# Kernel tuning notes

Measured on AMD Instinct MI355X. Metric: run time of the kernel, lower is better.

Reference implementation:

```python
import jax, jax.numpy as jnp
import numpy as np

NODES = 14      # input_size: nodes per graph
IN_F = 24       # seq_len: node feature dim
HID1 = 32
HID2 = 64       # hid_feats
HEADS = 2
OUT = 24        # output_size
B = 2048        # number of graphs
SLOPE = 0.2


def _make_edges():
    # fully connected (no self loops) within each 14-node graph
    pairs = np.array([(i, j) for i in range(NODES) for j in range(NODES) if i != j]).T  # [2,182]
    offs = (np.arange(B) * NODES)[:, None]
    src = (pairs[0][None, :] + offs).reshape(-1)
    dst = (pairs[1][None, :] + offs).reshape(-1)
    return np.stack([src, dst]).astype(np.int32)  # [2, 372736]


def setup_inputs() -> dict:
    key = jax.random.key(0)
    ks = jax.random.split(key, 16)
    N = B * NODES
    x = jax.random.normal(ks[0], (N, IN_F), dtype=jnp.float32)
    y = jax.random.normal(ks[1], (N, OUT), dtype=jnp.float32)
    edge_index = jnp.asarray(_make_edges())
    batch = jnp.repeat(jnp.arange(B, dtype=jnp.int32), NODES)
    s = 0.1
    params = dict(
        W1=jax.random.normal(ks[2], (IN_F, HEADS * HID1), dtype=jnp.float32) * s,
        a_src1=jax.random.normal(ks[3], (HEADS, HID1), dtype=jnp.float32) * s,
        a_dst1=jax.random.normal(ks[4], (HEADS, HID1), dtype=jnp.float32) * s,
        b1=jnp.zeros((HID1,), dtype=jnp.float32),
        W2=jax.random.normal(ks[5], (HID1, HEADS * HID2), dtype=jnp.float32) * s,
        a_src2=jax.random.normal(ks[6], (HEADS, HID2), dtype=jnp.float32) * s,
        a_dst2=jax.random.normal(ks[7], (HEADS, HID2), dtype=jnp.float32) * s,
        b2=jnp.zeros((HID2,), dtype=jnp.float32),
        Wf1=jax.random.normal(ks[8], (NODES, HID2, 8), dtype=jnp.float32) * s,
        bf1=jnp.zeros((NODES, 8), dtype=jnp.float32),
        Wf2=jax.random.normal(ks[9], (NODES, 8, OUT), dtype=jnp.float32) * s,
        bf2=jnp.zeros((NODES, OUT), dtype=jnp.float32),
    )
    return {"x": x, "y": y, "edge_index": edge_index, "batch": batch, **params}


def gat_conv(x, src, dst, W, a_src, a_dst, b):
    # PyG GATConv, concat=False (mean over heads), self-loops already in src/dst
    N = x.shape[0]
    H, F = a_src.shape
    xh = (x @ W).reshape(N, H, F)                       # [N,H,F]
    al_s = (xh * a_src).sum(-1)                         # [N,H]
    al_d = (xh * a_dst).sum(-1)                         # [N,H]
    alpha = jax.nn.leaky_relu(al_s[src] + al_d[dst], SLOPE)  # [E,H]
    amax = jax.ops.segment_max(alpha, dst, num_segments=N)
    ex = jnp.exp(alpha - amax[dst])
    den = jax.ops.segment_sum(ex, dst, num_segments=N)
    w = ex / den[dst]                                   # softmax per target node
    out = jax.ops.segment_sum(w[:, :, None] * xh[src], dst, num_segments=N)  # [N,H,F]
    return out.mean(axis=1) + b


def reference(x, y, edge_index, batch, W1, a_src1, a_dst1, b1, W2, a_src2, a_dst2, b2, Wf1, bf1, Wf2, bf2):
    N = x.shape[0]
    loops = jnp.arange(N, dtype=edge_index.dtype)
    src = jnp.concatenate([edge_index[0], loops])
    dst = jnp.concatenate([edge_index[1], loops])
    h = jax.nn.elu(gat_conv(x, src, dst, W1, a_src1, a_dst1, b1))   # [N,32]
    h = gat_conv(h, src, dst, W2, a_src2, a_dst2, b2)               # [N,64]
    # batch regroup: batch ids are contiguous per graph, so the Python
    # gather-loop in the original is exactly a reshape
    nb = N // NODES
    xg = h.reshape(nb, NODES, HID2).transpose(1, 0, 2)   # [14, B, 64]
    yg = y.reshape(nb, NODES, OUT)                       # [B, 14, out]
    # per-node-index MLP ensemble, batched over the 14 indices
    hh = jax.nn.relu(jnp.einsum('kbh,kho->kbo', xg, Wf1) + bf1[:, None, :])
    pred = jax.nn.sigmoid(jnp.einsum('kbo,kop->kbp', hh, Wf2) + bf2[:, None, :])  # [14,B,out]
    return pred, yg
```

## Files before the change

### kernel.cpp

```cpp
#include <hip/hip_runtime.h>

#define NODES 14
#define IN_F 24
#define HID1 32
#define HID2 64
#define OUT_F 24
#define SLOPE 0.2f

#define U_US1 0
#define U_UD1 48
#define U_US2 96
#define U_UD2 160

#define GPB 4
#define XS_S 28
#define H1_S 36
#define H2_S 68
#define WT_S 20
#define PHASE_FENCE() __builtin_amdgcn_sched_barrier(0)

__global__ __launch_bounds__(256) void compute_uvecs(
    const float* __restrict__ W1, const float* __restrict__ a_src1,
    const float* __restrict__ a_dst1,
    const float* __restrict__ W2, const float* __restrict__ a_src2,
    const float* __restrict__ a_dst2, float* __restrict__ u)
{
  const int tid = threadIdx.x;
  if (tid < 96) {
    const int sd = (tid >= 48), r = tid - sd * 48;
    const int h = (r >= IN_F), k = r - h * IN_F;
    const float* av = sd ? a_dst1 : a_src1;
    float s = 0.f;
#pragma unroll
    for (int f = 0; f < HID1; ++f)
      s += W1[k * 64 + h * HID1 + f] * av[h * HID1 + f];
    u[(sd ? U_UD1 : U_US1) + h * IN_F + k] = s;
  } else if (tid < 224) {
    const int j = tid - 96;
    const int sd = (j >= 64), r = j - sd * 64;
    const int h = (r >= HID1), k = r - h * HID1;
    const float* av = sd ? a_dst2 : a_src2;
    float s = 0.f;
#pragma unroll
    for (int f = 0; f < HID2; ++f)
      s += W2[k * 128 + h * HID2 + f] * av[h * HID2 + f];
    u[(sd ? U_UD2 : U_US2) + h * HID1 + k] = s;
  }
}

__global__ __launch_bounds__(64 * GPB) void gnn_fused(
    const float* __restrict__ x, const float* __restrict__ y,
    const float* __restrict__ W1, const float* __restrict__ b1,
    const float* __restrict__ W2, const float* __restrict__ b2,
    const float* __restrict__ Wf1, const float* __restrict__ bf1,
    const float* __restrict__ Wf2, const float* __restrict__ bf2,
    const float* __restrict__ uvec,
    float* __restrict__ out, int ngraphs)
{
  const int tid  = threadIdx.x;
  const int lane = tid & 63;
  const int wv   = tid >> 6;
  const int gu   = __builtin_amdgcn_readfirstlane(blockIdx.x * GPB + wv);
  if (gu >= ngraphs) return;

  __shared__ __align__(16) float xs[GPB][NODES * XS_S];
  __shared__ __align__(16) float h1s[GPB][NODES * H1_S];
  __shared__ __align__(16) float h2s[GPB][NODES * H2_S];
  __shared__ __align__(16) float wt[GPB][28 * WT_S];
  __shared__ __align__(16) float als[GPB][32];
  __shared__ __align__(16) float ald[GPB][32];
  __shared__ __align__(16) float hhs[GPB][120];

  const float* xg = x + (size_t)gu * (NODES * IN_F);

  float w1r[IN_F];
#pragma unroll
  for (int k = 0; k < IN_F; ++k) w1r[k] = W1[k * 64 + lane];
  float w2r[64];
#pragma unroll
  for (int k = 0; k < HID1; ++k) {
    w2r[k]      = W2[k * 128 + lane];
    w2r[32 + k] = W2[k * 128 + 64 + lane];
  }
  {
    const float4* x4 = (const float4*)xg;
#pragma unroll
    for (int i = lane; i < (NODES * IN_F) / 4; i += 64) {
      const float4 v = x4[i];
      const int n = (i * 4) / IN_F, k = (i * 4) - n * IN_F;
      *(float4*)&xs[wv][n * XS_S + k] = v;
    }
  }
  PHASE_FENCE();

  {
    const float4* y4 = (const float4*)(y + (size_t)gu * (NODES * OUT_F));
    float4* o4 = (float4*)(out + (size_t)NODES * ngraphs * OUT_F
                               + (size_t)gu * (NODES * OUT_F));
    for (int i = lane; i < (NODES * OUT_F) / 4; i += 64) o4[i] = y4[i];
  }

  float xcol[NODES];
#pragma unroll 2
  for (int n = 0; n < NODES; ++n) {
    float acc = 0.f;
#pragma unroll
    for (int k4 = 0; k4 < IN_F / 4; ++k4) {
      const float4 xv = *(const float4*)&xs[wv][n * XS_S + k4 * 4];
      acc += xv.x * w1r[k4 * 4 + 0] + xv.y * w1r[k4 * 4 + 1]
           + xv.z * w1r[k4 * 4 + 2] + xv.w * w1r[k4 * 4 + 3];
    }
    xcol[n] = acc;
  }

  if (lane < 56) {
    const int n = lane >> 2, h = (lane >> 1) & 1, sd = lane & 1;
    const float* uu = uvec + (sd ? U_UD1 : U_US1) + h * IN_F;
    float s = 0.f;
#pragma unroll
    for (int k4 = 0; k4 < 6; ++k4) {
      const float4 xv = *(const float4*)&xs[wv][n * XS_S + k4 * 4];
      const float4 uv = *(const float4*)&uu[k4 * 4];
      s += xv.x * uv.x + xv.y * uv.y + xv.z * uv.z + xv.w * uv.w;
    }
    (sd ? ald : als)[wv][h * 16 + n] = s;
  }
  if (lane < NODES * 2) {
    const int j = lane >> 1, h = lane & 1;
    const float ad = ald[wv][h * 16 + j];
    const float4 A0 = *(const float4*)&als[wv][h * 16 + 0];
    const float4 A1 = *(const float4*)&als[wv][h * 16 + 4];
    const float4 A2 = *(const float4*)&als[wv][h * 16 + 8];
    const float2 A3 = *(const float2*)&als[wv][h * 16 + 12];
    float a[NODES] = {A0.x, A0.y, A0.z, A0.w, A1.x, A1.y, A1.z, A1.w,
                      A2.x, A2.y, A2.z, A2.w, A3.x, A3.y};
    float m = -1e30f;
#pragma unroll
    for (int i = 0; i < NODES; ++i) {
      float v = a[i] + ad;
      v = v > 0.f ? v : SLOPE * v;
      a[i] = v; m = fmaxf(m, v);
    }
    float den = 0.f;
#pragma unroll
    for (int i = 0; i < NODES; ++i) { a[i] = __expf(a[i] - m); den += a[i]; }
    const float r = 1.f / den;
    float* wr = &wt[wv][(j * 2 + h) * WT_S];
    *(float4*)&wr[0]  = make_float4(a[0]*r,  a[1]*r,  a[2]*r,  a[3]*r);
    *(float4*)&wr[4]  = make_float4(a[4]*r,  a[5]*r,  a[6]*r,  a[7]*r);
    *(float4*)&wr[8]  = make_float4(a[8]*r,  a[9]*r,  a[10]*r, a[11]*r);
    *(float2*)&wr[12] = make_float2(a[12]*r, a[13]*r);
  }

  {
    const int h = lane >> 5, f5 = lane & 31;
    const float bb = b1[f5];
#pragma unroll 2
    for (int n = 0; n < NODES; ++n) {
      const float* wr = &wt[wv][(n * 2 + h) * WT_S];
      const float4 w0 = *(const float4*)&wr[0];
      const float4 w1 = *(const float4*)&wr[4];
      const float4 w2 = *(const float4*)&wr[8];
      const float2 w3 = *(const float2*)&wr[12];
      float o = w0.x*xcol[0] + w0.y*xcol[1] + w0.z*xcol[2] + w0.w*xcol[3]
              + w1.x*xcol[4] + w1.y*xcol[5] + w1.z*xcol[6] + w1.w*xcol[7]
              + w2.x*xcol[8] + w2.y*xcol[9] + w2.z*xcol[10] + w2.w*xcol[11]
              + w3.x*xcol[12] + w3.y*xcol[13];
      const float oo = __shfl_xor(o, 32);
      if (h == 0) {
        const float v = 0.5f * (o + oo) + bb;
        h1s[wv][n * H1_S + f5] = v > 0.f ? v : expm1f(v);
      }
    }
  }
  PHASE_FENCE();

  float acc0[NODES], acc1[NODES];
#pragma unroll 2
  for (int n = 0; n < NODES; ++n) {
    const float4 v0 = *(const float4*)&h1s[wv][n * H1_S + 0];
    const float4 v1 = *(const float4*)&h1s[wv][n * H1_S + 4];
    const float4 v2 = *(const float4*)&h1s[wv][n * H1_S + 8];
    const float4 v3 = *(const float4*)&h1s[wv][n * H1_S + 12];
    const float4 v4 = *(const float4*)&h1s[wv][n * H1_S + 16];
    const float4 v5 = *(const float4*)&h1s[wv][n * H1_S + 20];
    const float4 v6 = *(const float4*)&h1s[wv][n * H1_S + 24];
    const float4 v7 = *(const float4*)&h1s[wv][n * H1_S + 28];
    acc0[n] = v0.x*w2r[0] + v0.y*w2r[1] + v0.z*w2r[2] + v0.w*w2r[3]
            + v1.x*w2r[4] + v1.y*w2r[5] + v1.z*w2r[6] + v1.w*w2r[7]
            + v2.x*w2r[8] + v2.y*w2r[9] + v2.z*w2r[10] + v2.w*w2r[11]
            + v3.x*w2r[12] + v3.y*w2r[13] + v3.z*w2r[14] + v3.w*w2r[15]
            + v4.x*w2r[16] + v4.y*w2r[17] + v4.z*w2r[18] + v4.w*w2r[19]
            + v5.x*w2r[20] + v5.y*w2r[21] + v5.z*w2r[22] + v5.w*w2r[23]
            + v6.x*w2r[24] + v6.y*w2r[25] + v6.z*w2r[26] + v6.w*w2r[27]
            + v7.x*w2r[28] + v7.y*w2r[29] + v7.z*w2r[30] + v7.w*w2r[31];
    acc1[n] = v0.x*w2r[32] + v0.y*w2r[33] + v0.z*w2r[34] + v0.w*w2r[35]
            + v1.x*w2r[36] + v1.y*w2r[37] + v1.z*w2r[38] + v1.w*w2r[39]
            + v2.x*w2r[40] + v2.y*w2r[41] + v2.z*w2r[42] + v2.w*w2r[43]
            + v3.x*w2r[44] + v3.y*w2r[45] + v3.z*w2r[46] + v3.w*w2r[47]
            + v4.x*w2r[48] + v4.y*w2r[49] + v4.z*w2r[50] + v4.w*w2r[51]
            + v5.x*w2r[52] + v5.y*w2r[53] + v5.z*w2r[54] + v5.w*w2r[55]
            + v6.x*w2r[56] + v6.y*w2r[57] + v6.z*w2r[58] + v6.w*w2r[59]
            + v7.x*w2r[60] + v7.y*w2r[61] + v7.z*w2r[62] + v7.w*w2r[63];
  }

  if (lane < 56) {
    const int n = lane >> 2, h = (lane >> 1) & 1, sd = lane & 1;
    const float* uu = uvec + (sd ? U_UD2 : U_US2) + h * HID1;
    float s = 0.f;
#pragma unroll
    for (int k4 = 0; k4 < 8; ++k4) {
      const float4 hv = *(const float4*)&h1s[wv][n * H1_S + k4 * 4];
      const float4 uv = *(const float4*)&uu[k4 * 4];
      s += hv.x * uv.x + hv.y * uv.y + hv.z * uv.z + hv.w * uv.w;
    }
    (sd ? ald : als)[wv][h * 16 + n] = s;
  }
  if (lane < NODES * 2) {
    const int j = lane >> 1, h = lane & 1;
    const float ad = ald[wv][h * 16 + j];
    const float4 A0 = *(const float4*)&als[wv][h * 16 + 0];
    const float4 A1 = *(const float4*)&als[wv][h * 16 + 4];
    const float4 A2 = *(const float4*)&als[wv][h * 16 + 8];
    const float2 A3 = *(const float2*)&als[wv][h * 16 + 12];
    float a[NODES] = {A0.x, A0.y, A0.z, A0.w, A1.x, A1.y, A1.z, A1.w,
                      A2.x, A2.y, A2.z, A2.w, A3.x, A3.y};
    float m = -1e30f;
#pragma unroll
    for (int i = 0; i < NODES; ++i) {
      float v = a[i] + ad;
      v = v > 0.f ? v : SLOPE * v;
      a[i] = v; m = fmaxf(m, v);
    }
    float den = 0.f;
#pragma unroll
    for (int i = 0; i < NODES; ++i) { a[i] = __expf(a[i] - m); den += a[i]; }
    const float r = 1.f / den;
    float* wr = &wt[wv][(j * 2 + h) * WT_S];
    *(float4*)&wr[0]  = make_float4(a[0]*r,  a[1]*r,  a[2]*r,  a[3]*r);
    *(float4*)&wr[4]  = make_float4(a[4]*r,  a[5]*r,  a[6]*r,  a[7]*r);
    *(float4*)&wr[8]  = make_float4(a[8]*r,  a[9]*r,  a[10]*r, a[11]*r);
    *(float2*)&wr[12] = make_float2(a[12]*r, a[13]*r);
  }

  {
    const float bb = b2[lane];
#pragma unroll 2
    for (int n = 0; n < NODES; ++n) {
      const float* wr0 = &wt[wv][(n * 2 + 0) * WT_S];
      const float* wr1 = &wt[wv][(n * 2 + 1) * WT_S];
      const float4 p0 = *(const float4*)&wr0[0];
      const float4 p1 = *(const float4*)&wr0[4];
      const float4 p2 = *(const float4*)&wr0[8];
      const float2 p3 = *(const float2*)&wr0[12];
      const float4 q0 = *(const float4*)&wr1[0];
      const float4 q1 = *(const float4*)&wr1[4];
      const float4 q2 = *(const float4*)&wr1[8];
      const float2 q3 = *(const float2*)&wr1[12];
      const float o0 = p0.x*acc0[0] + p0.y*acc0[1] + p0.z*acc0[2] + p0.w*acc0[3]
                     + p1.x*acc0[4] + p1.y*acc0[5] + p1.z*acc0[6] + p1.w*acc0[7]
                     + p2.x*acc0[8] + p2.y*acc0[9] + p2.z*acc0[10] + p2.w*acc0[11]
                     + p3.x*acc0[12] + p3.y*acc0[13];
      const float o1 = q0.x*acc1[0] + q0.y*acc1[1] + q0.z*acc1[2] + q0.w*acc1[3]
                     + q1.x*acc1[4] + q1.y*acc1[5] + q1.z*acc1[6] + q1.w*acc1[7]
                     + q2.x*acc1[8] + q2.y*acc1[9] + q2.z*acc1[10] + q2.w*acc1[11]
                     + q3.x*acc1[12] + q3.y*acc1[13];
      h2s[wv][n * H2_S + lane] = 0.5f * (o0 + o1) + bb;
    }
  }
  PHASE_FENCE();

  if (lane < 56) {
    const int k = lane >> 2, e2 = (lane & 3) * 2;
    float a0 = bf1[k * 8 + e2], a1 = bf1[k * 8 + e2 + 1];
#pragma unroll
    for (int f4 = 0; f4 < 16; ++f4) {
      const float4 hv = *(const float4*)&h2s[wv][k * H2_S + f4 * 4];
      const float2 wa = *(const float2*)&Wf1[(k * HID2 + f4 * 4 + 0) * 8 + e2];
      const float2 wb = *(const float2*)&Wf1[(k * HID2 + f4 * 4 + 1) * 8 + e2];
      const float2 wc = *(const float2*)&Wf1[(k * HID2 + f4 * 4 + 2) * 8 + e2];
      const float2 wd = *(const float2*)&Wf1[(k * HID2 + f4 * 4 + 3) * 8 + e2];
      a0 += hv.x * wa.x + hv.y * wb.x + hv.z * wc.x + hv.w * wd.x;
      a1 += hv.x * wa.y + hv.y * wb.y + hv.z * wc.y + hv.w * wd.y;
    }
    *(float2*)&hhs[wv][k * 8 + e2] =
        make_float2(fmaxf(a0, 0.f), fmaxf(a1, 0.f));
  }

  for (int idx = lane; idx < NODES * (OUT_F / 4); idx += 64) {
    const int k = idx / (OUT_F / 4), o4 = (idx - k * (OUT_F / 4)) * 4;
    const float4 h0 = *(const float4*)&hhs[wv][k * 8];
    const float4 h1 = *(const float4*)&hhs[wv][k * 8 + 4];
    float4 acc = *(const float4*)&bf2[k * OUT_F + o4];
    const float he[8] = {h0.x, h0.y, h0.z, h0.w, h1.x, h1.y, h1.z, h1.w};
#pragma unroll
    for (int e = 0; e < 8; ++e) {
      const float4 wv4 = *(const float4*)&Wf2[(k * 8 + e) * OUT_F + o4];
      acc.x += he[e] * wv4.x; acc.y += he[e] * wv4.y;
      acc.z += he[e] * wv4.z; acc.w += he[e] * wv4.w;
    }
    acc.x = 1.f / (1.f + __expf(-acc.x));
    acc.y = 1.f / (1.f + __expf(-acc.y));
    acc.z = 1.f / (1.f + __expf(-acc.z));
    acc.w = 1.f / (1.f + __expf(-acc.w));
    *(float4*)&out[(size_t)k * ngraphs * OUT_F + (size_t)gu * OUT_F + o4] = acc;
  }
}

extern "C" void kernel_launch(void* const* d_in, const int* in_sizes, int n_in,
                              void* d_out, int out_size, void* d_ws, size_t ws_size,
                              hipStream_t stream) {
  const float* x      = (const float*)d_in[0];
  const float* y      = (const float*)d_in[1];
  const float* W1     = (const float*)d_in[4];
  const float* a_src1 = (const float*)d_in[5];
  const float* a_dst1 = (const float*)d_in[6];
  const float* b1     = (const float*)d_in[7];
  const float* W2     = (const float*)d_in[8];
  const float* a_src2 = (const float*)d_in[9];
  const float* a_dst2 = (const float*)d_in[10];
  const float* b2     = (const float*)d_in[11];
  const float* Wf1    = (const float*)d_in[12];
  const float* bf1    = (const float*)d_in[13];
  const float* Wf2    = (const float*)d_in[14];
  const float* bf2    = (const float*)d_in[15];
  float* out = (float*)d_out;
  float* u   = (float*)d_ws;

  const int nnodes  = in_sizes[0] / IN_F;
  const int ngraphs = nnodes / NODES;
  const int nblocks = (ngraphs + GPB - 1) / GPB;

  hipLaunchKernelGGL(compute_uvecs, dim3(1), dim3(256), 0, stream,
                     W1, a_src1, a_dst1, W2, a_src2, a_dst2, u);
  hipLaunchKernelGGL(gnn_fused, dim3(nblocks), dim3(64 * GPB), 0, stream,
                     x, y, W1, b1, W2, b2, Wf1, bf1, Wf2, bf2, u, out, ngraphs);
}
```

Measured before the change: 30.53 us.

## Drop precompute kernel; compute attention logits via wave shuffles in fused kernel

Removes the separate single-block kernel that folded the attention vectors into the weights, so only one kernel is launched. The attention source and destination logits are now computed from the already-projected features with cross-lane shuffle reductions instead of from LDS-staged inputs. Node features are read straight from global memory rather than staged in LDS, which also drops several shared buffers. In exchange the code issues many more shuffle instructions (log-step reductions per node for both layers) and scalar global reads of x.

```diff
diff --git a/kernel.cpp b/kernel.cpp
--- a/kernel.cpp
+++ b/kernel.cpp
@@ -7,54 +7,20 @@
 #define OUT_F 24
 #define SLOPE 0.2f
 
-#define U_US1 0
-#define U_UD1 48
-#define U_US2 96
-#define U_UD2 160
-
 #define GPB 4
-#define XS_S 28
 #define H1_S 36
 #define H2_S 68
 #define WT_S 20
 #define PHASE_FENCE() __builtin_amdgcn_sched_barrier(0)
 
-__global__ __launch_bounds__(256) void compute_uvecs(
-    const float* __restrict__ W1, const float* __restrict__ a_src1,
-    const float* __restrict__ a_dst1,
-    const float* __restrict__ W2, const float* __restrict__ a_src2,
-    const float* __restrict__ a_dst2, float* __restrict__ u)
-{
-  const int tid = threadIdx.x;
-  if (tid < 96) {
-    const int sd = (tid >= 48), r = tid - sd * 48;
-    const int h = (r >= IN_F), k = r - h * IN_F;
-    const float* av = sd ? a_dst1 : a_src1;
-    float s = 0.f;
-#pragma unroll
-    for (int f = 0; f < HID1; ++f)
-      s += W1[k * 64 + h * HID1 + f] * av[h * HID1 + f];
-    u[(sd ? U_UD1 : U_US1) + h * IN_F + k] = s;
-  } else if (tid < 224) {
-    const int j = tid - 96;
-    const int sd = (j >= 64), r = j - sd * 64;
-    const int h = (r >= HID1), k = r - h * HID1;
-    const float* av = sd ? a_dst2 : a_src2;
-    float s = 0.f;
-#pragma unroll
-    for (int f = 0; f < HID2; ++f)
-      s += W2[k * 128 + h * HID2 + f] * av[h * HID2 + f];
-    u[(sd ? U_UD2 : U_US2) + h * HID1 + k] = s;
-  }
-}
-
 __global__ __launch_bounds__(64 * GPB) void gnn_fused(
     const float* __restrict__ x, const float* __restrict__ y,
-    const float* __restrict__ W1, const float* __restrict__ b1,
-    const float* __restrict__ W2, const float* __restrict__ b2,
+    const float* __restrict__ W1, const float* __restrict__ a_src1,
+    const float* __restrict__ a_dst1, const float* __restrict__ b1,
+    const float* __restrict__ W2, const float* __restrict__ a_src2,
+    const float* __restrict__ a_dst2, const float* __restrict__ b2,
     const float* __restrict__ Wf1, const float* __restrict__ bf1,
     const float* __restrict__ Wf2, const float* __restrict__ bf2,
-    const float* __restrict__ uvec,
     float* __restrict__ out, int ngraphs)
 {
   const int tid  = threadIdx.x;
@@ -63,12 +29,9 @@
   const int gu   = __builtin_amdgcn_readfirstlane(blockIdx.x * GPB + wv);
   if (gu >= ngraphs) return;
 
-  __shared__ __align__(16) float xs[GPB][NODES * XS_S];
   __shared__ __align__(16) float h1s[GPB][NODES * H1_S];
   __shared__ __align__(16) float h2s[GPB][NODES * H2_S];
   __shared__ __align__(16) float wt[GPB][28 * WT_S];
-  __shared__ __align__(16) float als[GPB][32];
-  __shared__ __align__(16) float ald[GPB][32];
   __shared__ __align__(16) float hhs[GPB][120];
 
   const float* xg = x + (size_t)gu * (NODES * IN_F);
@@ -82,15 +45,12 @@
     w2r[k]      = W2[k * 128 + lane];
     w2r[32 + k] = W2[k * 128 + 64 + lane];
   }
-  {
-    const float4* x4 = (const float4*)xg;
-#pragma unroll
-    for (int i = lane; i < (NODES * IN_F) / 4; i += 64) {
-      const float4 v = x4[i];
-      const int n = (i * 4) / IN_F, k = (i * 4) - n * IN_F;
-      *(float4*)&xs[wv][n * XS_S + k] = v;
-    }
-  }
+  const float as1  = a_src1[lane];
+  const float ad1v = a_dst1[lane];
+  const float as2a = a_src2[lane];
+  const float as2b = a_src2[64 + lane];
+  const float ad2a = a_dst2[lane];
+  const float ad2b = a_dst2[64 + lane];
   PHASE_FENCE();
 
   {
@@ -105,39 +65,32 @@
   for (int n = 0; n < NODES; ++n) {
     float acc = 0.f;
 #pragma unroll
-    for (int k4 = 0; k4 < IN_F / 4; ++k4) {
-      const float4 xv = *(const float4*)&xs[wv][n * XS_S + k4 * 4];
-      acc += xv.x * w1r[k4 * 4 + 0] + xv.y * w1r[k4 * 4 + 1]
-           + xv.z * w1r[k4 * 4 + 2] + xv.w * w1r[k4 * 4 + 3];
-    }
+    for (int k = 0; k < IN_F; ++k) acc += xg[n * IN_F + k] * w1r[k];
     xcol[n] = acc;
   }
 
-  if (lane < 56) {
-    const int n = lane >> 2, h = (lane >> 1) & 1, sd = lane & 1;
-    const float* uu = uvec + (sd ? U_UD1 : U_US1) + h * IN_F;
-    float s = 0.f;
-#pragma unroll
-    for (int k4 = 0; k4 < 6; ++k4) {
-      const float4 xv = *(const float4*)&xs[wv][n * XS_S + k4 * 4];
-      const float4 uv = *(const float4*)&uu[k4 * 4];
-      s += xv.x * uv.x + xv.y * uv.y + xv.z * uv.z + xv.w * uv.w;
-    }
-    (sd ? ald : als)[wv][h * 16 + n] = s;
-  }
-  if (lane < NODES * 2) {
-    const int j = lane >> 1, h = lane & 1;
-    const float ad = ald[wv][h * 16 + j];
-    const float4 A0 = *(const float4*)&als[wv][h * 16 + 0];
-    const float4 A1 = *(const float4*)&als[wv][h * 16 + 4];
-    const float4 A2 = *(const float4*)&als[wv][h * 16 + 8];
-    const float2 A3 = *(const float2*)&als[wv][h * 16 + 12];
-    float a[NODES] = {A0.x, A0.y, A0.z, A0.w, A1.x, A1.y, A1.z, A1.w,
-                      A2.x, A2.y, A2.z, A2.w, A3.x, A3.y};
-    float m = -1e30f;
+  float alsr[NODES], aldr[NODES];
+#pragma unroll
+  for (int n = 0; n < NODES; ++n) {
+    float s = xcol[n] * as1, d = xcol[n] * ad1v;
+#pragma unroll
+    for (int off = 1; off < 32; off <<= 1) {
+      s += __shfl_xor(s, off);
+      d += __shfl_xor(d, off);
+    }
+    alsr[n] = s; aldr[n] = d;
+  }
+
+  const int h = lane >> 5, f5 = lane & 31;
+
+  if (f5 < NODES) {
+    float ad = aldr[0];
+#pragma unroll
+    for (int i = 1; i < NODES; ++i) ad = (f5 == i) ? aldr[i] : ad;
+    float a[NODES]; float m = -1e30f;
 #pragma unroll
     for (int i = 0; i < NODES; ++i) {
-      float v = a[i] + ad;
+      float v = alsr[i] + ad;
       v = v > 0.f ? v : SLOPE * v;
       a[i] = v; m = fmaxf(m, v);
     }
@@ -145,7 +98,7 @@
 #pragma unroll
     for (int i = 0; i < NODES; ++i) { a[i] = __expf(a[i] - m); den += a[i]; }
     const float r = 1.f / den;
-    float* wr = &wt[wv][(j * 2 + h) * WT_S];
+    float* wr = &wt[wv][(f5 * 2 + h) * WT_S];
     *(float4*)&wr[0]  = make_float4(a[0]*r,  a[1]*r,  a[2]*r,  a[3]*r);
     *(float4*)&wr[4]  = make_float4(a[4]*r,  a[5]*r,  a[6]*r,  a[7]*r);
     *(float4*)&wr[8]  = make_float4(a[8]*r,  a[9]*r,  a[10]*r, a[11]*r);
@@ -153,7 +106,6 @@
   }
 
   {
-    const int h = lane >> 5, f5 = lane & 31;
     const float bb = b1[f5];
 #pragma unroll 2
     for (int n = 0; n < NODES; ++n) {
@@ -204,31 +156,30 @@
             + v7.x*w2r[60] + v7.y*w2r[61] + v7.z*w2r[62] + v7.w*w2r[63];
   }
 
-  if (lane < 56) {
-    const int n = lane >> 2, h = (lane >> 1) & 1, sd = lane & 1;
-    const float* uu = uvec + (sd ? U_UD2 : U_US2) + h * HID1;
-    float s = 0.f;
-#pragma unroll
-    for (int k4 = 0; k4 < 8; ++k4) {
-      const float4 hv = *(const float4*)&h1s[wv][n * H1_S + k4 * 4];
-      const float4 uv = *(const float4*)&uu[k4 * 4];
-      s += hv.x * uv.x + hv.y * uv.y + hv.z * uv.z + hv.w * uv.w;
-    }
-    (sd ? ald : als)[wv][h * 16 + n] = s;
-  }
-  if (lane < NODES * 2) {
-    const int j = lane >> 1, h = lane & 1;
-    const float ad = ald[wv][h * 16 + j];
-    const float4 A0 = *(const float4*)&als[wv][h * 16 + 0];
-    const float4 A1 = *(const float4*)&als[wv][h * 16 + 4];
-    const float4 A2 = *(const float4*)&als[wv][h * 16 + 8];
-    const float2 A3 = *(const float2*)&als[wv][h * 16 + 12];
-    float a[NODES] = {A0.x, A0.y, A0.z, A0.w, A1.x, A1.y, A1.z, A1.w,
-                      A2.x, A2.y, A2.z, A2.w, A3.x, A3.y};
-    float m = -1e30f;
+  float als2r[NODES], ald2r[NODES];
+#pragma unroll
+  for (int n = 0; n < NODES; ++n) {
+    float s0 = acc0[n] * as2a, s1 = acc1[n] * as2b;
+    float d0 = acc0[n] * ad2a, d1 = acc1[n] * ad2b;
+#pragma unroll
+    for (int off = 1; off < 64; off <<= 1) {
+      s0 += __shfl_xor(s0, off);
+      s1 += __shfl_xor(s1, off);
+      d0 += __shfl_xor(d0, off);
+      d1 += __shfl_xor(d1, off);
+    }
+    als2r[n] = h ? s1 : s0;
+    ald2r[n] = h ? d1 : d0;
+  }
+
+  if (f5 < NODES) {
+    float ad = ald2r[0];
+#pragma unroll
+    for (int i = 1; i < NODES; ++i) ad = (f5 == i) ? ald2r[i] : ad;
+    float a[NODES]; float m = -1e30f;
 #pragma unroll
     for (int i = 0; i < NODES; ++i) {
-      float v = a[i] + ad;
+      float v = als2r[i] + ad;
       v = v > 0.f ? v : SLOPE * v;
       a[i] = v; m = fmaxf(m, v);
     }
@@ -236,7 +187,7 @@
 #pragma unroll
     for (int i = 0; i < NODES; ++i) { a[i] = __expf(a[i] - m); den += a[i]; }
     const float r = 1.f / den;
-    float* wr = &wt[wv][(j * 2 + h) * WT_S];
+    float* wr = &wt[wv][(f5 * 2 + h) * WT_S];
     *(float4*)&wr[0]  = make_float4(a[0]*r,  a[1]*r,  a[2]*r,  a[3]*r);
     *(float4*)&wr[4]  = make_float4(a[4]*r,  a[5]*r,  a[6]*r,  a[7]*r);
     *(float4*)&wr[8]  = make_float4(a[8]*r,  a[9]*r,  a[10]*r, a[11]*r);
@@ -290,9 +241,9 @@
   for (int idx = lane; idx < NODES * (OUT_F / 4); idx += 64) {
     const int k = idx / (OUT_F / 4), o4 = (idx - k * (OUT_F / 4)) * 4;
     const float4 h0 = *(const float4*)&hhs[wv][k * 8];
-    const float4 h1 = *(const float4*)&hhs[wv][k * 8 + 4];
+    const float4 hq = *(const float4*)&hhs[wv][k * 8 + 4];
     float4 acc = *(const float4*)&bf2[k * OUT_F + o4];
-    const float he[8] = {h0.x, h0.y, h0.z, h0.w, h1.x, h1.y, h1.z, h1.w};
+    const float he[8] = {h0.x, h0.y, h0.z, h0.w, hq.x, hq.y, hq.z, hq.w};
 #pragma unroll
     for (int e = 0; e < 8; ++e) {
       const float4 wv4 = *(const float4*)&Wf2[(k * 8 + e) * OUT_F + o4];
@@ -325,14 +276,12 @@
   const float* Wf2    = (const float*)d_in[14];
   const float* bf2    = (const float*)d_in[15];
   float* out = (float*)d_out;
-  float* u   = (float*)d_ws;
 
   const int nnodes  = in_sizes[0] / IN_F;
   const int ngraphs = nnodes / NODES;
   const int nblocks = (ngraphs + GPB - 1) / GPB;
 
-  hipLaunchKernelGGL(compute_uvecs, dim3(1), dim3(256), 0, stream,
-                     W1, a_src1, a_dst1, W2, a_src2, a_dst2, u);
   hipLaunchKernelGGL(gnn_fused, dim3(nblocks), dim3(64 * GPB), 0, stream,
-                     x, y, W1, b1, W2, b2, Wf1, bf1, Wf2, bf2, u, out, ngraphs);
+                     x, y, W1, a_src1, a_dst1, b1, W2, a_src2, a_dst2, b2,
+                     Wf1, bf1, Wf2, bf2, out, ngraphs);
 }
```

New measurement: 31.82 us. 4.2% more time.
